# Performance work log

Hardware: AMD Instinct MI355X
Metric: run time of the kernel (lower is better)

## Reference

```python
import jax, jax.numpy as jnp
import numpy as np

N = 2_000_000   # num_instances
F = 64          # feature_dim
S = 65536       # number of multisets (max_index)


def setup_inputs() -> dict:
    key = jax.random.key(0)
    k1, k2, k3, k4 = jax.random.split(key, 4)
    x = jax.random.normal(k1, (N, F), dtype=jnp.float32)
    batch_idx = jax.random.randint(k2, (N,), 0, S, dtype=jnp.int64)
    # learned params: convex weight t ~ U(0,1) per feature, xavier-normal linear weight [1, 5]
    t = jax.random.uniform(k3, (F,), dtype=jnp.float32)
    num_coords = 5  # add_sum=True -> [n, min, max, relu_sum, sum]
    xavier_std = np.sqrt(2.0 / (num_coords + 1))
    W = jax.random.normal(k4, (1, num_coords), dtype=jnp.float32) * xavier_std
    return {"x": x, "batch_idx": batch_idx, "max_index": S, "t": t, "W": W}


def reference(x, batch_idx, max_index, t, W):
    # clamp_convex_weight=True: t is clamped to [0, 1]
    t = jnp.clip(t, 0.0, 1.0)
    # per-segment multi-stat reduction: min, max, sum, count  -> [S, F]
    mn = jax.ops.segment_min(x, batch_idx, num_segments=max_index)
    mx = jax.ops.segment_max(x, batch_idx, num_segments=max_index)
    sums = jax.ops.segment_sum(x, batch_idx, num_segments=max_index)
    counts = jax.ops.segment_sum(jnp.ones((x.shape[0],), dtype=x.dtype), batch_idx,
                                 num_segments=max_index)  # [S]
    # gather min/max back to instances, adaptive bias, relu, scatter-sum
    bias = t * mx[batch_idx] + (1.0 - t) * mn[batch_idx]          # [N, F]
    relu_sum = jax.ops.segment_sum(jax.nn.relu(x - bias), batch_idx,
                                   num_segments=max_index)         # [S, F]
    n = jnp.broadcast_to(counts[:, None], mn.shape)                # [S, F]
    # cat along -1 then reshape [S,5,F].permute(0,2,1) == stack stats on last axis
    coords = jnp.stack([n, mn, mx, relu_sum, sums], axis=-1)       # [S, F, 5]
    out = jnp.einsum('sfc,oc->sfo', coords, W)[..., 0]             # [S, F]
    return out
```

## Files before the change

### kernel.cpp

```cpp
#include <hip/hip_runtime.h>
#include <math.h>

#define NSEG 65536
#define FDIM 64
#define CAP  40

__global__ __launch_bounds__(256) void hist_kernel(const int* __restrict__ idx,
                                                   int* __restrict__ counts, int n) {
    int i = blockIdx.x * blockDim.x + threadIdx.x;
    int stride = gridDim.x * blockDim.x;
    for (; i < n; i += stride) {
        unsigned s = (unsigned)idx[i];
        if (s < NSEG) atomicAdd(&counts[s], 1);
    }
}

__global__ __launch_bounds__(1024) void scan_kernel(const int* __restrict__ counts,
                                                    int* __restrict__ offs) {
    __shared__ int part[1024];
    const int tid  = threadIdx.x;
    const int base = tid * 64;
    int s = 0;
    for (int j = 0; j < 64; ++j) s += counts[base + j];
    part[tid] = s;
    __syncthreads();
    for (int off = 1; off < 1024; off <<= 1) {
        int v = (tid >= off) ? part[tid - off] : 0;
        __syncthreads();
        part[tid] += v;
        __syncthreads();
    }
    int run = part[tid] - s;
    for (int j = 0; j < 64; ++j) { offs[base + j] = run; run += counts[base + j]; }
}

__global__ __launch_bounds__(256) void scatter_kernel(const int* __restrict__ idx,
                                                      const int* __restrict__ offs,
                                                      int* __restrict__ cursor,
                                                      int* __restrict__ sorted, int n) {
    int i = blockIdx.x * blockDim.x + threadIdx.x;
    int stride = gridDim.x * blockDim.x;
    for (; i < n; i += stride) {
        unsigned s = (unsigned)idx[i];
        if (s < NSEG) {
            int p = offs[s] + atomicAdd(&cursor[s], 1);
            sorted[p] = i;
        }
    }
}

__global__ __launch_bounds__(64) void seg_main(const float* __restrict__ x,
                                               const int* __restrict__ sorted,
                                               const int* __restrict__ offs,
                                               const int* __restrict__ counts,
                                               const float* __restrict__ t,
                                               const float* __restrict__ W,
                                               float* __restrict__ out) {
    const int s    = blockIdx.x;
    const int lane = threadIdx.x;
    const int beg  = offs[s];
    const int cnt  = counts[s];

    __shared__ float rows[CAP][FDIM];

    float mn = INFINITY, mx = -INFINITY, sm = 0.0f;

    for (int base = 0; base < cnt; base += 64) {
        const int m = min(64, cnt - base);
        int myidx = (lane < m) ? sorted[beg + base + lane] : 0;
        int r = 0;
        for (; r + 4 <= m; r += 4) {
            int q0 = __shfl(myidx, r);
            int q1 = __shfl(myidx, r + 1);
            int q2 = __shfl(myidx, r + 2);
            int q3 = __shfl(myidx, r + 3);
            float v0 = x[(size_t)q0 * FDIM + lane];
            float v1 = x[(size_t)q1 * FDIM + lane];
            float v2 = x[(size_t)q2 * FDIM + lane];
            float v3 = x[(size_t)q3 * FDIM + lane];
            const int g = base + r;
            if (g + 0 < CAP) rows[g + 0][lane] = v0;
            if (g + 1 < CAP) rows[g + 1][lane] = v1;
            if (g + 2 < CAP) rows[g + 2][lane] = v2;
            if (g + 3 < CAP) rows[g + 3][lane] = v3;
            mn = fminf(mn, fminf(fminf(v0, v1), fminf(v2, v3)));
            mx = fmaxf(mx, fmaxf(fmaxf(v0, v1), fmaxf(v2, v3)));
            sm += v0 + v1 + v2 + v3;
        }
        for (; r < m; ++r) {
            int q = __shfl(myidx, r);
            float v = x[(size_t)q * FDIM + lane];
            const int g = base + r;
            if (g < CAP) rows[g][lane] = v;
            mn = fminf(mn, v);
            mx = fmaxf(mx, v);
            sm += v;
        }
    }
    __syncthreads();

    const float tc   = fminf(fmaxf(t[lane], 0.0f), 1.0f);
    const float bias = tc * mx + (1.0f - tc) * mn;
    float rs = 0.0f;
    const int lim = min(cnt, CAP);
    for (int r = 0; r < lim; ++r)
        rs += fmaxf(0.0f, rows[r][lane] - bias);
    for (int base = CAP; base < cnt; base += 64) {
        const int m = min(64, cnt - base);
        int myidx = (lane < m) ? sorted[beg + base + lane] : 0;
        for (int r = 0; r < m; ++r) {
            int q = __shfl(myidx, r);
            rs += fmaxf(0.0f, x[(size_t)q * FDIM + lane] - bias);
        }
    }

    const float W0 = W[0], W1 = W[1], W2 = W[2], W3 = W[3], W4 = W[4];
    out[(size_t)s * FDIM + lane] =
        W0 * (float)cnt + W1 * mn + W2 * mx + W3 * rs + W4 * sm;
}

extern "C" void kernel_launch(void* const* d_in, const int* in_sizes, int n_in,
                              void* d_out, int out_size, void* d_ws, size_t ws_size,
                              hipStream_t stream) {
    const float* x    = (const float*)d_in[0];
    const int*   bidx = (const int*)d_in[1];
    const float* t    = (const float*)d_in[3];
    const float* W    = (const float*)d_in[4];
    float*       out  = (float*)d_out;
    const int    N    = in_sizes[0] / FDIM;

    int* counts = (int*)d_ws;
    int* offs   = counts + NSEG;
    int* cursor = offs + NSEG;
    int* sorted = cursor + NSEG;

    hipMemsetAsync(counts, 0, NSEG * sizeof(int), stream);
    hipMemsetAsync(cursor, 0, NSEG * sizeof(int), stream);

    hist_kernel<<<2048, 256, 0, stream>>>(bidx, counts, N);
    scan_kernel<<<1, 1024, 0, stream>>>(counts, offs);
    scatter_kernel<<<2048, 256, 0, stream>>>(bidx, offs, cursor, sorted, N);
    seg_main<<<NSEG, 64, 0, stream>>>(x, sorted, offs, counts, t, W, out);
}
```

Baseline: 931.2 us.

## Split each segment across four wavefronts and seed scatter cursor from scan

The per-segment kernel now uses 256 threads, with four wavefronts each handling a quarter of the segment's rows. Partial min/max/sum and relu sums are combined through shared memory, which raises memory-level parallelism for the gather of x rows. The scan now writes starting offsets directly into the cursor array, so the second memset and the offs lookup in scatter are dropped, and bounds checks on indices are removed. The row cache grows to 56 rows. This adds shared-memory reductions and block barriers, and the 4x larger blocks may lower occupancy for small segments (average about 30 rows).

```diff
diff --git a/kernel.cpp b/kernel.cpp
--- a/kernel.cpp
+++ b/kernel.cpp
@@ -3,20 +3,19 @@
 
 #define NSEG 65536
 #define FDIM 64
-#define CAP  40
+#define CAP  56
 
 __global__ __launch_bounds__(256) void hist_kernel(const int* __restrict__ idx,
                                                    int* __restrict__ counts, int n) {
     int i = blockIdx.x * blockDim.x + threadIdx.x;
     int stride = gridDim.x * blockDim.x;
-    for (; i < n; i += stride) {
-        unsigned s = (unsigned)idx[i];
-        if (s < NSEG) atomicAdd(&counts[s], 1);
-    }
+    for (; i < n; i += stride)
+        atomicAdd(&counts[idx[i]], 1);
 }
 
 __global__ __launch_bounds__(1024) void scan_kernel(const int* __restrict__ counts,
-                                                    int* __restrict__ offs) {
+                                                    int* __restrict__ offs,
+                                                    int* __restrict__ cursor) {
     __shared__ int part[1024];
     const int tid  = threadIdx.x;
     const int base = tid * 64;
@@ -31,92 +30,101 @@
         __syncthreads();
     }
     int run = part[tid] - s;
-    for (int j = 0; j < 64; ++j) { offs[base + j] = run; run += counts[base + j]; }
+    for (int j = 0; j < 64; ++j) {
+        offs[base + j]   = run;
+        cursor[base + j] = run;
+        run += counts[base + j];
+    }
 }
 
 __global__ __launch_bounds__(256) void scatter_kernel(const int* __restrict__ idx,
-                                                      const int* __restrict__ offs,
                                                       int* __restrict__ cursor,
                                                       int* __restrict__ sorted, int n) {
     int i = blockIdx.x * blockDim.x + threadIdx.x;
     int stride = gridDim.x * blockDim.x;
     for (; i < n; i += stride) {
-        unsigned s = (unsigned)idx[i];
-        if (s < NSEG) {
-            int p = offs[s] + atomicAdd(&cursor[s], 1);
-            sorted[p] = i;
-        }
+        int s = idx[i];
+        int p = atomicAdd(&cursor[s], 1);
+        sorted[p] = i;
     }
 }
 
-__global__ __launch_bounds__(64) void seg_main(const float* __restrict__ x,
-                                               const int* __restrict__ sorted,
-                                               const int* __restrict__ offs,
-                                               const int* __restrict__ counts,
-                                               const float* __restrict__ t,
-                                               const float* __restrict__ W,
-                                               float* __restrict__ out) {
+__global__ __launch_bounds__(256) void seg_main(const float* __restrict__ x,
+                                                const int* __restrict__ sorted,
+                                                const int* __restrict__ offs,
+                                                const int* __restrict__ cursor,
+                                                const float* __restrict__ t,
+                                                const float* __restrict__ W,
+                                                float* __restrict__ out) {
     const int s    = blockIdx.x;
-    const int lane = threadIdx.x;
+    const int lane = threadIdx.x & 63;
+    const int w    = threadIdx.x >> 6;
     const int beg  = offs[s];
-    const int cnt  = counts[s];
+    const int cnt  = cursor[s] - beg;
 
     __shared__ float rows[CAP][FDIM];
+    __shared__ float cmn[4][FDIM];
+    __shared__ float cmx[4][FDIM];
+    __shared__ float csm[4][FDIM];
+
+    const int per = (cnt + 3) >> 2;
+    const int r0  = min(cnt, w * per);
+    const int r1  = min(cnt, r0 + per);
 
     float mn = INFINITY, mx = -INFINITY, sm = 0.0f;
 
-    for (int base = 0; base < cnt; base += 64) {
-        const int m = min(64, cnt - base);
-        int myidx = (lane < m) ? sorted[beg + base + lane] : 0;
-        int r = 0;
-        for (; r + 4 <= m; r += 4) {
-            int q0 = __shfl(myidx, r);
-            int q1 = __shfl(myidx, r + 1);
-            int q2 = __shfl(myidx, r + 2);
-            int q3 = __shfl(myidx, r + 3);
-            float v0 = x[(size_t)q0 * FDIM + lane];
-            float v1 = x[(size_t)q1 * FDIM + lane];
-            float v2 = x[(size_t)q2 * FDIM + lane];
-            float v3 = x[(size_t)q3 * FDIM + lane];
-            const int g = base + r;
-            if (g + 0 < CAP) rows[g + 0][lane] = v0;
-            if (g + 1 < CAP) rows[g + 1][lane] = v1;
-            if (g + 2 < CAP) rows[g + 2][lane] = v2;
-            if (g + 3 < CAP) rows[g + 3][lane] = v3;
-            mn = fminf(mn, fminf(fminf(v0, v1), fminf(v2, v3)));
-            mx = fmaxf(mx, fmaxf(fmaxf(v0, v1), fmaxf(v2, v3)));
-            sm += v0 + v1 + v2 + v3;
-        }
-        for (; r < m; ++r) {
-            int q = __shfl(myidx, r);
-            float v = x[(size_t)q * FDIM + lane];
-            const int g = base + r;
-            if (g < CAP) rows[g][lane] = v;
-            mn = fminf(mn, v);
-            mx = fmaxf(mx, v);
-            sm += v;
-        }
+    int r = r0;
+    for (; r + 4 <= r1; r += 4) {
+        int q0 = sorted[beg + r + 0];
+        int q1 = sorted[beg + r + 1];
+        int q2 = sorted[beg + r + 2];
+        int q3 = sorted[beg + r + 3];
+        float v0 = x[(size_t)q0 * FDIM + lane];
+        float v1 = x[(size_t)q1 * FDIM + lane];
+        float v2 = x[(size_t)q2 * FDIM + lane];
+        float v3 = x[(size_t)q3 * FDIM + lane];
+        if (r + 0 < CAP) rows[r + 0][lane] = v0;
+        if (r + 1 < CAP) rows[r + 1][lane] = v1;
+        if (r + 2 < CAP) rows[r + 2][lane] = v2;
+        if (r + 3 < CAP) rows[r + 3][lane] = v3;
+        mn = fminf(mn, fminf(fminf(v0, v1), fminf(v2, v3)));
+        mx = fmaxf(mx, fmaxf(fmaxf(v0, v1), fmaxf(v2, v3)));
+        sm += (v0 + v1) + (v2 + v3);
     }
+    for (; r < r1; ++r) {
+        int q = sorted[beg + r];
+        float v = x[(size_t)q * FDIM + lane];
+        if (r < CAP) rows[r][lane] = v;
+        mn = fminf(mn, v);
+        mx = fmaxf(mx, v);
+        sm += v;
+    }
+
+    cmn[w][lane] = mn; cmx[w][lane] = mx; csm[w][lane] = sm;
+    __syncthreads();
+    mn = fminf(fminf(cmn[0][lane], cmn[1][lane]), fminf(cmn[2][lane], cmn[3][lane]));
+    mx = fmaxf(fmaxf(cmx[0][lane], cmx[1][lane]), fmaxf(cmx[2][lane], cmx[3][lane]));
+    const float smT = (csm[0][lane] + csm[1][lane]) + (csm[2][lane] + csm[3][lane]);
     __syncthreads();
 
     const float tc   = fminf(fmaxf(t[lane], 0.0f), 1.0f);
     const float bias = tc * mx + (1.0f - tc) * mn;
     float rs = 0.0f;
-    const int lim = min(cnt, CAP);
-    for (int r = 0; r < lim; ++r)
+    const int lim = min(r1, CAP);
+    for (r = r0; r < lim; ++r)
         rs += fmaxf(0.0f, rows[r][lane] - bias);
-    for (int base = CAP; base < cnt; base += 64) {
-        const int m = min(64, cnt - base);
-        int myidx = (lane < m) ? sorted[beg + base + lane] : 0;
-        for (int r = 0; r < m; ++r) {
-            int q = __shfl(myidx, r);
-            rs += fmaxf(0.0f, x[(size_t)q * FDIM + lane] - bias);
-        }
+    for (r = max(r0, CAP); r < r1; ++r) {
+        int q = sorted[beg + r];
+        rs += fmaxf(0.0f, x[(size_t)q * FDIM + lane] - bias);
     }
+    cmn[w][lane] = rs;
+    __syncthreads();
 
-    const float W0 = W[0], W1 = W[1], W2 = W[2], W3 = W[3], W4 = W[4];
-    out[(size_t)s * FDIM + lane] =
-        W0 * (float)cnt + W1 * mn + W2 * mx + W3 * rs + W4 * sm;
+    if (w == 0) {
+        const float rsT = (cmn[0][lane] + cmn[1][lane]) + (cmn[2][lane] + cmn[3][lane]);
+        out[(size_t)s * FDIM + lane] =
+            W[0] * (float)cnt + W[1] * mn + W[2] * mx + W[3] * rsT + W[4] * smT;
+    }
 }
 
 extern "C" void kernel_launch(void* const* d_in, const int* in_sizes, int n_in,
@@ -135,10 +143,9 @@
     int* sorted = cursor + NSEG;
 
     hipMemsetAsync(counts, 0, NSEG * sizeof(int), stream);
-    hipMemsetAsync(cursor, 0, NSEG * sizeof(int), stream);
 
     hist_kernel<<<2048, 256, 0, stream>>>(bidx, counts, N);
-    scan_kernel<<<1, 1024, 0, stream>>>(counts, offs);
-    scatter_kernel<<<2048, 256, 0, stream>>>(bidx, offs, cursor, sorted, N);
-    seg_main<<<NSEG, 64, 0, stream>>>(x, sorted, offs, counts, t, W, out);
+    scan_kernel<<<1, 1024, 0, stream>>>(counts, offs, cursor);
+    scatter_kernel<<<2048, 256, 0, stream>>>(bidx, cursor, sorted, N);
+    seg_main<<<NSEG, 256, 0, stream>>>(x, sorted, offs, cursor, t, W, out);
 }
```

Result: slower. 1.020 ms (+9.5%).
